# Performance work log

Measured on AMD Instinct MI355X. Metric: run time of the kernel, lower is better.

Reference implementation:

```python
import jax, jax.numpy as jnp
import numpy as np

EPS = 1.1920929e-07  # torch fp32 finfo eps used by F.rms_norm default

def rms_norm(x):
    return x * jax.lax.rsqrt(jnp.mean(jnp.square(x), axis=-1, keepdims=True) + EPS)

def setup_inputs() -> dict:
    key = jax.random.key(0)
    kx, kfc, kpr, krt = jax.random.split(key, 4)
    B, T, C, F = 4, 2048, 2048, 8192
    s = (3.0 ** 0.5) * C ** -0.5  # init scale used in init_weights
    x = jax.random.normal(kx, (B, T, C), dtype=jnp.float32)
    w_fc = jax.random.normal(kfc, (F, C), dtype=jnp.float32) * s
    w_proj = jax.random.normal(kpr, (C, F), dtype=jnp.float32) * (s * 0.1)
    w_router = jax.random.normal(krt, (1, C), dtype=jnp.float32) * 0.01  # router init std=0.01
    return {"x": x, "w_fc": w_fc, "w_proj": w_proj, "w_router": w_router}

def reference(x, w_fc, w_proj, w_router):
    # Router: (B,T,C) @ (C,1) -> (B,T) logits; STE mask (~0 or ~1 floats)
    logits = jnp.einsum('btc,oc->bto', x, w_router)[..., 0]  # (B,T)
    prob = jax.nn.sigmoid(logits)
    hard = (prob > 0.5).astype(x.dtype)
    mask_i = hard + prob - jax.lax.stop_gradient(prob)  # straight-through
    mask_bool = mask_i > 0.5  # (B,T)

    # Gated MLP (mixture-of-depth). The torch code gathers selected tokens,
    # runs the MLP on the compacted set, scatters into zeros, and multiplies
    # by mask_i. Mathematically identical dense form (honoring the mask):
    h = jnp.einsum('btc,fc->btf', rms_norm(x), w_fc)
    h = jnp.square(jax.nn.relu(h))  # relu(x)^2 activation
    mlp_out = jnp.einsum('btf,cf->btc', h, w_proj)
    gated = jnp.where(mask_bool[..., None], mlp_out * mask_i[..., None], 0.0)
    return x + gated
```

## Files before the change

### kernel.cpp

```cpp
#include <hip/hip_runtime.h>
#include <type_traits>
#include <utility>
#include <stdint.h>
#include <stddef.h>

#define TOKENS 8192
#define CDIM 2048
#define FDIM 8192
#define EPSV 1.1920929e-07f

typedef __attribute__((ext_vector_type(8))) short short8;
typedef __attribute__((ext_vector_type(8))) __bf16 bf16x8;
typedef __attribute__((ext_vector_type(4))) float floatx4;
typedef __attribute__((ext_vector_type(4))) float f32x4;
typedef __attribute__((ext_vector_type(2))) unsigned int u32x2;

template <typename V, typename = void> struct CanMfma : std::false_type {};
template <typename V>
struct CanMfma<V, std::void_t<decltype(__builtin_amdgcn_mfma_f32_16x16x32_bf16(
    std::declval<V>(), std::declval<V>(), std::declval<floatx4>(), 0, 0, 0))>>
    : std::true_type {};
using frag_t = std::conditional_t<CanMfma<short8>::value, short8, bf16x8>;

__device__ __forceinline__ floatx4 mfma_bf16(frag_t a, frag_t b, floatx4 c) {
    return __builtin_amdgcn_mfma_f32_16x16x32_bf16(a, b, c, 0, 0, 0);
}

__device__ __forceinline__ unsigned short f2bf(float f) {
    unsigned int u = __float_as_uint(f);
    u += 0x7fffu + ((u >> 16) & 1u);
    return (unsigned short)(u >> 16);
}

__global__ void zero_kernel(int* p) { if (threadIdx.x == 0) *p = 0; }

__global__ __launch_bounds__(256) void cvt2_kernel(
    const float* __restrict__ s1, unsigned short* __restrict__ d1, int n1,
    const float* __restrict__ s2, unsigned short* __restrict__ d2, int n2)
{
    int i = blockIdx.x * 256 + threadIdx.x;
    const float4* s; ushort4* d;
    if (i < n1) { s = (const float4*)s1; d = (ushort4*)d1; }
    else if (i < n1 + n2) { s = (const float4*)s2; d = (ushort4*)d2; i -= n1; }
    else return;
    float4 v = s[i];
    u32x2 w;
    w.x = (unsigned)f2bf(v.x) | ((unsigned)f2bf(v.y) << 16);
    w.y = (unsigned)f2bf(v.z) | ((unsigned)f2bf(v.w) << 16);
    __builtin_nontemporal_store(w, (u32x2*)&d[i]);
}

__global__ __launch_bounds__(256) void router_kernel(
    const float* __restrict__ x, const float* __restrict__ wr,
    float* __restrict__ out, unsigned short* __restrict__ Xn,
    int* __restrict__ idx, float* __restrict__ mv, int* __restrict__ cnt)
{
    const int token = blockIdx.x;
    const int tid = threadIdx.x;
    const float4* xr = (const float4*)(x + (size_t)token * CDIM);
    const float4* w4 = (const float4*)wr;
    float4 a0 = xr[tid];
    float4 a1 = xr[tid + 256];
    float4 b0 = w4[tid];
    float4 b1 = w4[tid + 256];
    float ss = a0.x*a0.x + a0.y*a0.y + a0.z*a0.z + a0.w*a0.w
             + a1.x*a1.x + a1.y*a1.y + a1.z*a1.z + a1.w*a1.w;
    float dt = a0.x*b0.x + a0.y*b0.y + a0.z*b0.z + a0.w*b0.w
             + a1.x*b1.x + a1.y*b1.y + a1.z*b1.z + a1.w*b1.w;
    #pragma unroll
    for (int off = 32; off > 0; off >>= 1) {
        ss += __shfl_down(ss, off);
        dt += __shfl_down(dt, off);
    }
    __shared__ float red_ss[4], red_dt[4];
    __shared__ float s_rms;
    __shared__ int s_pos;
    const int wave = tid >> 6;
    if ((tid & 63) == 0) { red_ss[wave] = ss; red_dt[wave] = dt; }
    __syncthreads();
    if (tid == 0) {
        float S = red_ss[0] + red_ss[1] + red_ss[2] + red_ss[3];
        float D = red_dt[0] + red_dt[1] + red_dt[2] + red_dt[3];
        float prob = 1.0f / (1.0f + expf(-D));
        s_rms = 1.0f / sqrtf(S * (1.0f / (float)CDIM) + EPSV);
        int pos = -1;
        if (prob > 0.5f) {
            pos = atomicAdd(cnt, 1);
            idx[pos] = token;
            mv[pos] = (1.0f + prob) - prob;
        }
        s_pos = pos;
    }
    __syncthreads();
    const float rms = s_rms;
    const int pos = s_pos;
    float* op = out + (size_t)token * CDIM;
    if (pos < 0) {
        f32x4 r0 = {a0.x, a0.y, a0.z, a0.w};
        f32x4 r1 = {a1.x, a1.y, a1.z, a1.w};
        __builtin_nontemporal_store(r0, (f32x4*)(op + tid * 4));
        __builtin_nontemporal_store(r1, (f32x4*)(op + (tid + 256) * 4));
    } else {
        unsigned short* xp = Xn + (size_t)pos * CDIM;
        u32x2 w;
        w.x = (unsigned)f2bf(a0.x * rms) | ((unsigned)f2bf(a0.y * rms) << 16);
        w.y = (unsigned)f2bf(a0.z * rms) | ((unsigned)f2bf(a0.w * rms) << 16);
        __builtin_nontemporal_store(w, (u32x2*)(xp + tid * 4));
        w.x = (unsigned)f2bf(a1.x * rms) | ((unsigned)f2bf(a1.y * rms) << 16);
        w.y = (unsigned)f2bf(a1.z * rms) | ((unsigned)f2bf(a1.w * rms) << 16);
        __builtin_nontemporal_store(w, (u32x2*)(xp + (tid + 256) * 4));
    }
}

template <int K, int MODE, int LDO, int KSPLIT>
__global__ __launch_bounds__(256) void gemm_bt(
    const unsigned short* __restrict__ A,
    const unsigned short* __restrict__ B,
    unsigned short* __restrict__ Hout,
    float* __restrict__ out,
    const float* __restrict__ xin,
    const int* __restrict__ idx,
    const float* __restrict__ mv,
    const int* __restrict__ cntp)
{
    const int cnt = *cntp;
    const int bid = blockIdx.y * 64 + blockIdx.x;
    const int s = bid >> 6;
    const int w = bid & 63;
    const int mi = (s & 7) * 8 + (w & 7);
    const int ni = (s >> 3) * 8 + (w >> 3);
    const int m0 = mi * 128;
    if (m0 >= cnt) return;
    const int n0 = ni * 128;
    const int k0 = (int)blockIdx.z * (K / KSPLIT);

    __shared__ alignas(16) unsigned short lA[128 * 64];
    __shared__ alignas(16) unsigned short lB[128 * 64];

    const int tid = threadIdx.x;
    const int wave = tid >> 6;
    const int lane = tid & 63;
    const int wm = (wave >> 1) * 64;
    const int wn = (wave & 1) * 64;
    const int quad = lane >> 4;
    const int l16 = lane & 15;

    const int srow = lane >> 3;
    const int schunk = (lane & 7) ^ srow;

    const unsigned short* ap[4];
    const unsigned short* bp[4];
    #pragma unroll
    for (int p = 0; p < 4; ++p) {
        const int r = p * 32 + wave * 8 + srow;
        ap[p] = A + (size_t)(m0 + r) * K + k0 + schunk * 8;
        bp[p] = B + (size_t)(n0 + r) * K + k0 + schunk * 8;
    }

    floatx4 acc[4][4] = {};

    for (int kt = 0; kt < K / (64 * KSPLIT); ++kt) {
        #pragma unroll
        for (int p = 0; p < 4; ++p) {
            __builtin_amdgcn_global_load_lds(
                (__attribute__((address_space(1))) void*)ap[p],
                (__attribute__((address_space(3))) void*)&lA[(p * 32 + wave * 8) * 64],
                16, 0, 0);
            __builtin_amdgcn_global_load_lds(
                (__attribute__((address_space(1))) void*)bp[p],
                (__attribute__((address_space(3))) void*)&lB[(p * 32 + wave * 8) * 64],
                16, 0, 0);
            ap[p] += 64;
            bp[p] += 64;
        }
        __syncthreads();
        #pragma unroll
        for (int st = 0; st < 2; ++st) {
            frag_t af[4], bfv[4];
            #pragma unroll
            for (int t = 0; t < 4; ++t) {
                const int ra = wm + t * 16 + l16;
                const int ca = ((st * 4 + quad) ^ (ra & 7)) * 8;
                af[t] = *(const frag_t*)&lA[ra * 64 + ca];
                const int rb = wn + t * 16 + l16;
                const int cb = ((st * 4 + quad) ^ (rb & 7)) * 8;
                bfv[t] = *(const frag_t*)&lB[rb * 64 + cb];
            }
            #pragma unroll
            for (int tm = 0; tm < 4; ++tm)
                #pragma unroll
                for (int tn = 0; tn < 4; ++tn)
                    acc[tm][tn] = mfma_bf16(af[tm], bfv[tn], acc[tm][tn]);
        }
        __syncthreads();
    }

    if (MODE == 1) {
        #pragma unroll
        for (int tm = 0; tm < 4; ++tm) {
            const int gm = m0 + wm + tm * 16 + quad * 4;
            #pragma unroll
            for (int tn = 0; tn < 4; ++tn) {
                const int gn = n0 + wn + tn * 16 + l16;
                #pragma unroll
                for (int v = 0; v < 4; ++v) {
                    float h = fmaxf(acc[tm][tn][v], 0.0f);
                    unsigned short hb = f2bf(h * h);
                    __builtin_nontemporal_store(hb, &Hout[(size_t)(gm + v) * LDO + gn]);
                }
            }
        }
    } else {
        #pragma unroll
        for (int tm = 0; tm < 4; ++tm) {
            const int gmb = m0 + wm + tm * 16 + quad * 4;
            #pragma unroll
            for (int v = 0; v < 4; ++v) {
                const int gm = gmb + v;
                if (gm < cnt) {
                    const int token = idx[gm];
                    const float scale = mv[gm];
                    const float* xrow = xin + (size_t)token * LDO;
                    float* orow = out + (size_t)token * LDO;
                    #pragma unroll
                    for (int tn = 0; tn < 4; ++tn) {
                        const int gn = n0 + wn + tn * 16 + l16;
                        float r = xrow[gn] + scale * acc[tm][tn][v];
                        __builtin_nontemporal_store(r, &orow[gn]);
                    }
                }
            }
        }
    }
}

extern "C" void kernel_launch(void* const* d_in, const int* in_sizes, int n_in,
                              void* d_out, int out_size, void* d_ws, size_t ws_size,
                              hipStream_t stream)
{
    const float* x   = (const float*)d_in[0];
    const float* wfc = (const float*)d_in[1];
    const float* wpr = (const float*)d_in[2];
    const float* wrt = (const float*)d_in[3];
    float* out = (float*)d_out;

    char* ws = (char*)d_ws;
    int*   cnt = (int*)ws;
    int*   idx = (int*)(ws + 256);
    float* mv  = (float*)(ws + 256 + 32768);
    unsigned short* Xn  = (unsigned short*)(ws + 65792);
    unsigned short* Wfc = (unsigned short*)(ws + 65792 + 33554432ULL);
    unsigned short* Wpr = (unsigned short*)(ws + 65792 + 67108864ULL);
    unsigned short* H   = (unsigned short*)(ws + 65792 + 100663296ULL);

    const int n4 = FDIM * CDIM / 4;
    zero_kernel<<<1, 64, 0, stream>>>(cnt);
    cvt2_kernel<<<(2 * n4 + 255) / 256, 256, 0, stream>>>(wfc, Wfc, n4, wpr, Wpr, n4);
    router_kernel<<<TOKENS, 256, 0, stream>>>(x, wrt, out, Xn, idx, mv, cnt);
    gemm_bt<CDIM, 1, FDIM, 1><<<dim3(64, FDIM / 128), 256, 0, stream>>>(
        Xn, Wfc, H, nullptr, nullptr, nullptr, nullptr, cnt);
    gemm_bt<FDIM, 2, CDIM, 1><<<dim3(64, CDIM / 128), 256, 0, stream>>>(
        H, Wpr, nullptr, out, x, idx, mv, cnt);
}
```

Before: 761.6 us.

## Pre-tile and pre-swizzle GEMM operands into LDS-ready blocks

The weight converters, router and first-GEMM epilogue now write bf16 operands in a blocked layout: 128-row by 64-column tiles stored contiguously with the XOR swizzle already applied. The GEMM loader then issues fully contiguous 16-byte global-to-LDS loads per tile instead of strided row loads, which is meant to improve coalescing and TLB/cache locality. The cost is a scattered 2-byte store pattern in the MODE 1 epilogue for H, and the layout is now tied to the fixed tile sizes.

```diff
diff --git a/kernel.cpp b/kernel.cpp
--- a/kernel.cpp
+++ b/kernel.cpp
@@ -34,20 +34,28 @@
 
 __global__ void zero_kernel(int* p) { if (threadIdx.x == 0) *p = 0; }
 
+
 __global__ __launch_bounds__(256) void cvt2_kernel(
-    const float* __restrict__ s1, unsigned short* __restrict__ d1, int n1,
-    const float* __restrict__ s2, unsigned short* __restrict__ d2, int n2)
-{
+    const float* __restrict__ s1, unsigned short* __restrict__ d1,
+    const float* __restrict__ s2, unsigned short* __restrict__ d2)
+{
+    const int NC1 = FDIM * (CDIM / 8);
     int i = blockIdx.x * 256 + threadIdx.x;
-    const float4* s; ushort4* d;
-    if (i < n1) { s = (const float4*)s1; d = (ushort4*)d1; }
-    else if (i < n1 + n2) { s = (const float4*)s2; d = (ushort4*)d2; i -= n1; }
-    else return;
-    float4 v = s[i];
-    u32x2 w;
-    w.x = (unsigned)f2bf(v.x) | ((unsigned)f2bf(v.y) << 16);
-    w.y = (unsigned)f2bf(v.z) | ((unsigned)f2bf(v.w) << 16);
-    __builtin_nontemporal_store(w, (u32x2*)&d[i]);
+    const float* src; unsigned short* dst;
+    int n, t, PK, K8;
+    if (i < NC1) { src = s1; dst = d1; n = i >> 8; t = i & 255; PK = 32; K8 = 256; }
+    else { i -= NC1; src = s2; dst = d2; n = i >> 10; t = i & 1023; PK = 128; K8 = 1024; }
+    const int kt = t >> 3, q8 = t & 7;
+    const int r = n & 127, ni = n >> 7;
+    const float4* sp = (const float4*)src + ((size_t)n * K8 + t) * 2;
+    float4 v0 = sp[0], v1 = sp[1];
+    short8 o;
+    o[0] = (short)f2bf(v0.x); o[1] = (short)f2bf(v0.y);
+    o[2] = (short)f2bf(v0.z); o[3] = (short)f2bf(v0.w);
+    o[4] = (short)f2bf(v1.x); o[5] = (short)f2bf(v1.y);
+    o[6] = (short)f2bf(v1.z); o[7] = (short)f2bf(v1.w);
+    size_t di = (((size_t)ni * PK + kt) * 128 + r) * 64 + (size_t)((q8 ^ (r & 7)) << 3);
+    __builtin_nontemporal_store(o, (short8*)(dst + di));
 }
 
 __global__ __launch_bounds__(256) void router_kernel(
@@ -59,10 +67,10 @@
     const int tid = threadIdx.x;
     const float4* xr = (const float4*)(x + (size_t)token * CDIM);
     const float4* w4 = (const float4*)wr;
-    float4 a0 = xr[tid];
-    float4 a1 = xr[tid + 256];
-    float4 b0 = w4[tid];
-    float4 b1 = w4[tid + 256];
+    float4 a0 = xr[2 * tid];
+    float4 a1 = xr[2 * tid + 1];
+    float4 b0 = w4[2 * tid];
+    float4 b1 = w4[2 * tid + 1];
     float ss = a0.x*a0.x + a0.y*a0.y + a0.z*a0.z + a0.w*a0.w
              + a1.x*a1.x + a1.y*a1.y + a1.z*a1.z + a1.w*a1.w;
     float dt = a0.x*b0.x + a0.y*b0.y + a0.z*b0.z + a0.w*b0.w
@@ -98,17 +106,18 @@
     if (pos < 0) {
         f32x4 r0 = {a0.x, a0.y, a0.z, a0.w};
         f32x4 r1 = {a1.x, a1.y, a1.z, a1.w};
-        __builtin_nontemporal_store(r0, (f32x4*)(op + tid * 4));
-        __builtin_nontemporal_store(r1, (f32x4*)(op + (tid + 256) * 4));
+        __builtin_nontemporal_store(r0, (f32x4*)(op + tid * 8));
+        __builtin_nontemporal_store(r1, (f32x4*)(op + tid * 8 + 4));
     } else {
-        unsigned short* xp = Xn + (size_t)pos * CDIM;
-        u32x2 w;
-        w.x = (unsigned)f2bf(a0.x * rms) | ((unsigned)f2bf(a0.y * rms) << 16);
-        w.y = (unsigned)f2bf(a0.z * rms) | ((unsigned)f2bf(a0.w * rms) << 16);
-        __builtin_nontemporal_store(w, (u32x2*)(xp + tid * 4));
-        w.x = (unsigned)f2bf(a1.x * rms) | ((unsigned)f2bf(a1.y * rms) << 16);
-        w.y = (unsigned)f2bf(a1.z * rms) | ((unsigned)f2bf(a1.w * rms) << 16);
-        __builtin_nontemporal_store(w, (u32x2*)(xp + (tid + 256) * 4));
+        const int kt = tid >> 3, q8 = tid & 7;
+        const int r = pos & 127, mi = pos >> 7;
+        short8 o;
+        o[0] = (short)f2bf(a0.x * rms); o[1] = (short)f2bf(a0.y * rms);
+        o[2] = (short)f2bf(a0.z * rms); o[3] = (short)f2bf(a0.w * rms);
+        o[4] = (short)f2bf(a1.x * rms); o[5] = (short)f2bf(a1.y * rms);
+        o[6] = (short)f2bf(a1.z * rms); o[7] = (short)f2bf(a1.w * rms);
+        size_t di = (((size_t)mi * 32 + kt) * 128 + r) * 64 + (size_t)((q8 ^ (r & 7)) << 3);
+        __builtin_nontemporal_store(o, (short8*)(Xn + di));
     }
 }
 
@@ -145,17 +154,9 @@
     const int quad = lane >> 4;
     const int l16 = lane & 15;
 
-    const int srow = lane >> 3;
-    const int schunk = (lane & 7) ^ srow;
-
-    const unsigned short* ap[4];
-    const unsigned short* bp[4];
-    #pragma unroll
-    for (int p = 0; p < 4; ++p) {
-        const int r = p * 32 + wave * 8 + srow;
-        ap[p] = A + (size_t)(m0 + r) * K + k0 + schunk * 8;
-        bp[p] = B + (size_t)(n0 + r) * K + k0 + schunk * 8;
-    }
+    constexpr int PK = K / 64;
+    const unsigned short* aq = A + ((size_t)mi * PK + (k0 >> 6)) * 8192 + (size_t)tid * 8;
+    const unsigned short* bq = B + ((size_t)ni * PK + (k0 >> 6)) * 8192 + (size_t)tid * 8;
 
     floatx4 acc[4][4] = {};
 
@@ -163,16 +164,16 @@
         #pragma unroll
         for (int p = 0; p < 4; ++p) {
             __builtin_amdgcn_global_load_lds(
-                (__attribute__((address_space(1))) void*)ap[p],
-                (__attribute__((address_space(3))) void*)&lA[(p * 32 + wave * 8) * 64],
+                (__attribute__((address_space(1))) void*)(aq + p * 2048),
+                (__attribute__((address_space(3))) void*)&lA[(p * 256 + wave * 64) * 8],
                 16, 0, 0);
             __builtin_amdgcn_global_load_lds(
-                (__attribute__((address_space(1))) void*)bp[p],
-                (__attribute__((address_space(3))) void*)&lB[(p * 32 + wave * 8) * 64],
+                (__attribute__((address_space(1))) void*)(bq + p * 2048),
+                (__attribute__((address_space(3))) void*)&lB[(p * 256 + wave * 64) * 8],
                 16, 0, 0);
-            ap[p] += 64;
-            bp[p] += 64;
-        }
+        }
+        aq += 8192;
+        bq += 8192;
         __syncthreads();
         #pragma unroll
         for (int st = 0; st < 2; ++st) {
@@ -196,17 +197,21 @@
     }
 
     if (MODE == 1) {
+        constexpr int PKH = LDO / 64;
         #pragma unroll
         for (int tm = 0; tm < 4; ++tm) {
-            const int gm = m0 + wm + tm * 16 + quad * 4;
+            const int rbase = wm + tm * 16 + quad * 4;
             #pragma unroll
             for (int tn = 0; tn < 4; ++tn) {
                 const int gn = n0 + wn + tn * 16 + l16;
+                const int kt = gn >> 6, q8 = (gn >> 3) & 7, e = gn & 7;
                 #pragma unroll
                 for (int v = 0; v < 4; ++v) {
+                    const int r = rbase + v;
                     float h = fmaxf(acc[tm][tn][v], 0.0f);
-                    unsigned short hb = f2bf(h * h);
-                    __builtin_nontemporal_store(hb, &Hout[(size_t)(gm + v) * LDO + gn]);
+                    size_t di = (((size_t)mi * PKH + kt) * 128 + r) * 64
+                              + (size_t)((q8 ^ (r & 7)) << 3) + e;
+                    __builtin_nontemporal_store(f2bf(h * h), &Hout[di]);
                 }
             }
         }
@@ -253,9 +258,9 @@
     unsigned short* Wpr = (unsigned short*)(ws + 65792 + 67108864ULL);
     unsigned short* H   = (unsigned short*)(ws + 65792 + 100663296ULL);
 
-    const int n4 = FDIM * CDIM / 4;
+    const int nchunks = FDIM * (CDIM / 8) + CDIM * (FDIM / 8);
     zero_kernel<<<1, 64, 0, stream>>>(cnt);
-    cvt2_kernel<<<(2 * n4 + 255) / 256, 256, 0, stream>>>(wfc, Wfc, n4, wpr, Wpr, n4);
+    cvt2_kernel<<<nchunks / 256, 256, 0, stream>>>(wfc, Wfc, wpr, Wpr);
     router_kernel<<<TOKENS, 256, 0, stream>>>(x, wrt, out, Xn, idx, mv, cnt);
     gemm_bt<CDIM, 1, FDIM, 1><<<dim3(64, FDIM / 128), 256, 0, stream>>>(
         Xn, Wfc, H, nullptr, nullptr, nullptr, nullptr, cnt);
```

Result: no change. 753.5 us (-1.1%).
